# Kernel tuning notes

Measured on AMD Instinct MI355X. Metric: run time of the kernel, lower is better.

## Reference

```python
import jax, jax.numpy as jnp
from jax import lax
import numpy as np

EPS = 1e-5
RADIUS = 0.2
NPOINT = 1024
NSAMPLE = 32
B, N = 8, 8192


def furthest_point_sample(xyz, npoint):
    # xyz: (B,N,3) -> idx (B,npoint), start at index 0 (pytorch3d default)
    Bn, Nn, _ = xyz.shape
    def step(carry, _):
        dists, last = carry  # (B,N), (B,)
        lastpt = jnp.take_along_axis(xyz, last[:, None, None], axis=1)  # (B,1,3)
        d = jnp.sum((xyz - lastpt) ** 2, axis=-1)  # (B,N)
        dists = jnp.minimum(dists, d)
        nxt = jnp.argmax(dists, axis=-1).astype(jnp.int32)
        return (dists, nxt), last
    init = (jnp.full((Bn, Nn), jnp.inf, xyz.dtype), jnp.zeros((Bn,), jnp.int32))
    _, idxs = lax.scan(step, init, None, length=npoint)  # (npoint,B)
    return idxs.T  # (B,npoint)


def ball_query(radius, nsample, xyz, new_xyz):
    # first `nsample` points (by original index order) within radius; pad -> 0 (clamp of -1)
    Nn = xyz.shape[1]
    d2 = jnp.sum((new_xyz[:, :, None, :] - xyz[:, None, :, :]) ** 2, axis=-1)  # (B,S,N)
    valid = d2 < radius * radius
    score = jnp.where(valid, jnp.arange(Nn, dtype=jnp.int32), jnp.int32(Nn))  # smaller = earlier valid
    neg_vals, _ = lax.top_k(-score, nsample)  # picks nsample smallest scores
    idx = -neg_vals  # (B,S,nsample)
    idx = jnp.where(idx == Nn, 0, idx)  # pytorch3d pads with -1, then clamp(min=0) -> 0
    return idx


def bn_relu(x, g, be, m, v):
    # eval-mode BatchNorm over channel (last) dim + ReLU
    return jax.nn.relu((x - m) * (g / jnp.sqrt(v + EPS)) + be)


def setup_inputs() -> dict:
    key = jax.random.key(0)
    ks = jax.random.split(key, 4)
    xyz = jax.random.uniform(ks[0], (B, N, 3), dtype=jnp.float32)
    w1 = jax.random.normal(ks[1], (64, 3), dtype=jnp.float32) * 0.1
    w2 = jax.random.normal(ks[2], (64, 64), dtype=jnp.float32) * 0.1
    w3 = jax.random.normal(ks[3], (128, 64), dtype=jnp.float32) * 0.1
    z64, o64 = jnp.zeros((64,), jnp.float32), jnp.ones((64,), jnp.float32)
    z128, o128 = jnp.zeros((128,), jnp.float32), jnp.ones((128,), jnp.float32)
    return {
        "xyz": xyz,
        "w1": w1, "b1": z64, "g1": o64, "be1": z64, "m1": z64, "v1": o64,
        "w2": w2, "b2": z64, "g2": o64, "be2": z64, "m2": z64, "v2": o64,
        "w3": w3, "b3": z128, "g3": o128, "be3": z128, "m3": z128, "v3": o128,
    }


def reference(xyz, w1, b1, g1, be1, m1, v1, w2, b2, g2, be2, m2, v2, w3, b3, g3, be3, m3, v3):
    fps_idx = furthest_point_sample(xyz, NPOINT)  # (B,npoint)
    new_xyz = jnp.take_along_axis(xyz, fps_idx[:, :, None], axis=1)  # (B,npoint,3)
    idx = ball_query(RADIUS, NSAMPLE, xyz, new_xyz)  # (B,npoint,nsample)
    grouped_xyz = jax.vmap(lambda pts, i: pts[i])(xyz, idx)  # (B,npoint,nsample,3)
    # 1x1 conv MLP (channels-last) + eval BN + ReLU
    h = bn_relu(jnp.einsum('bsnc,oc->bsno', grouped_xyz, w1) + b1, g1, be1, m1, v1)
    h = bn_relu(jnp.einsum('bsnc,oc->bsno', h, w2) + b2, g2, be2, m2, v2)
    h = bn_relu(jnp.einsum('bsnc,oc->bsno', h, w3) + b3, g3, be3, m3, v3)
    new_features = jnp.max(h, axis=2)  # (B,npoint,128) max over nsample
    new_features = jnp.transpose(new_features, (0, 2, 1))  # (B,128,npoint) to match torch layout
    return new_xyz, new_features
```

## Files before the change

kernel.cpp:

```cpp
#include <hip/hip_runtime.h>

#define B 8
#define N 8192
#define S 1024
#define NS 32
#define THREADS 512
#define NCONS_BLK 248
#define NCONS_WAVE (NCONS_BLK * 8)
constexpr float BN_EPS = 1e-5f;

typedef float v2f __attribute__((ext_vector_type(2)));

struct KParams {
  const float* xyz;
  const float *w1, *b1, *g1, *be1, *m1, *v1;
  const float *w2, *b2, *g2, *be2, *m2, *v2;
  const float *w3, *b3, *g3, *be3, *m3, *v3;
  float* new_xyz;
  float* out_feat;
  float* ctrs;
  unsigned* prog;
};

__device__ __forceinline__ float wave_max_to_lane63(float x) {
  int v = __float_as_int(x);
#define DPP_MAX(ctrl)                                                     \
  v = __float_as_int(fmaxf(__int_as_float(v),                             \
      __int_as_float(__builtin_amdgcn_update_dpp(v, v, (ctrl), 0xf, 0xf, \
                                                 false))))
  DPP_MAX(0x111);
  DPP_MAX(0x112);
  DPP_MAX(0x114);
  DPP_MAX(0x118);
  DPP_MAX(0x142);
  DPP_MAX(0x143);
#undef DPP_MAX
  return __int_as_float(v);
}

__device__ __forceinline__ void producer(const KParams& P, char* smem, int b,
                                         int t, int lane, int w) {
#pragma clang fp contract(off)
  float4* s_xyz4 = (float4*)smem;
  float* s_ctr = (float*)(smem + 131072);
  unsigned long long(*s_red)[8] =
      (unsigned long long(*)[8])(smem + 131072 + 12288);
  const float* base = P.xyz + (size_t)b * N * 3;
  v2f X[8], Y[8], Z[8], D[8];
  const int p0 = t * 16;
  {
    const float4* src = (const float4*)(base + (size_t)p0 * 3);
    float buf[48];
#pragma unroll
    for (int i = 0; i < 12; ++i) {
      float4 v = src[i];
      buf[4 * i + 0] = v.x; buf[4 * i + 1] = v.y;
      buf[4 * i + 2] = v.z; buf[4 * i + 3] = v.w;
    }
#pragma unroll
    for (int k = 0; k < 16; ++k)
      s_xyz4[p0 + k] =
          make_float4(buf[3 * k], buf[3 * k + 1], buf[3 * k + 2], 0.f);
#pragma unroll
    for (int i = 0; i < 8; ++i) {
      X[i] = (v2f){buf[6 * i + 0], buf[6 * i + 3]};
      Y[i] = (v2f){buf[6 * i + 1], buf[6 * i + 4]};
      Z[i] = (v2f){buf[6 * i + 2], buf[6 * i + 5]};
      D[i] = (v2f){3.4e38f, 3.4e38f};
    }
  }
  __syncthreads();
  float lx = base[0], ly = base[1], lz = base[2];
  if (t == 0) { s_ctr[0] = lx; s_ctr[1] = ly; s_ctr[2] = lz; }
  for (int r = 1; r < S; ++r) {
    v2f lx2 = lx, ly2 = ly, lz2 = lz;
#pragma unroll
    for (int i = 0; i < 8; ++i) {
      v2f dx = X[i] - lx2, dy = Y[i] - ly2, dz = Z[i] - lz2;
      v2f d = (dx * dx + dy * dy) + dz * dz;
      D[i] = __builtin_elementwise_min(D[i], d);
    }
    float n1[8], n2[4], n3[2];
#pragma unroll
    for (int i = 0; i < 8; ++i) n1[i] = fmaxf(D[i].x, D[i].y);
#pragma unroll
    for (int i = 0; i < 4; ++i) n2[i] = fmaxf(n1[2 * i], n1[2 * i + 1]);
    n3[0] = fmaxf(n2[0], n2[1]);
    n3[1] = fmaxf(n2[2], n2[3]);
    float m = fmaxf(n3[0], n3[1]);
    int c3 = (n3[0] < m) ? 1 : 0;
    float n2s = c3 ? n2[2] : n2[0];
    int c2 = (n2s < m) ? 1 : 0;
    float n1a = c3 ? n1[4] : n1[0];
    float n1b = c3 ? n1[6] : n1[2];
    float n1s = c2 ? n1b : n1a;
    int c1 = (n1s < m) ? 1 : 0;
    float dx0 = c3 ? D[4].x : D[0].x;
    float dx1 = c3 ? D[5].x : D[1].x;
    float dx2 = c3 ? D[6].x : D[2].x;
    float dx3 = c3 ? D[7].x : D[3].x;
    float dxa = c2 ? dx2 : dx0;
    float dxb = c2 ? dx3 : dx1;
    float dxs = c1 ? dxb : dxa;
    int c0 = (dxs < m) ? 1 : 0;
    int li = 8 * c3 + 4 * c2 + 2 * c1 + c0;
    float wm = wave_max_to_lane63(m);
    float wavemax =
        __int_as_float(__builtin_amdgcn_readlane(__float_as_int(wm), 63));
    unsigned long long bal = __ballot(m == wavemax);
    int firstlane = (int)__builtin_ctzll(bal);
    int widx = __builtin_amdgcn_readlane(p0 + li, firstlane);
    unsigned long long key =
        ((unsigned long long)__float_as_uint(wavemax) << 32) |
        (unsigned)(8191 - widx);
    if (lane == 0) s_red[r & 1][w] = key;
    __syncthreads();
    {
      const unsigned long long* sr = s_red[r & 1];
      unsigned long long k0 = sr[0], k1 = sr[1], k2 = sr[2], k3 = sr[3];
      unsigned long long k4 = sr[4], k5 = sr[5], k6 = sr[6], k7 = sr[7];
      unsigned long long a = k0 > k1 ? k0 : k1;
      unsigned long long c = k2 > k3 ? k2 : k3;
      unsigned long long e = k4 > k5 ? k4 : k5;
      unsigned long long g = k6 > k7 ? k6 : k7;
      unsigned long long ac = a > c ? a : c;
      unsigned long long eg = e > g ? e : g;
      unsigned long long kmax = ac > eg ? ac : eg;
      const int bi = 8191 - (int)(unsigned)(kmax & 0xffffffffull);
      float4 cc = s_xyz4[bi];
      lx = cc.x; ly = cc.y; lz = cc.z;
    }
    if (t == 0) {
      s_ctr[r * 3 + 0] = lx; s_ctr[r * 3 + 1] = ly; s_ctr[r * 3 + 2] = lz;
    }
    if (w == 0 && (r & 15) == 15) {
      int k16 = r >> 4;
      if (lane == 0 && k16 >= 1)
        __hip_atomic_store(&P.prog[b * 64], (unsigned)(k16 * 16),
                           __ATOMIC_RELEASE, __HIP_MEMORY_SCOPE_AGENT);
      int cbase = (r - 15) * 3;
      if (lane < 48)
        __hip_atomic_store(P.ctrs + (size_t)b * (S * 3) + cbase + lane,
                           s_ctr[cbase + lane], __ATOMIC_RELAXED,
                           __HIP_MEMORY_SCOPE_AGENT);
    }
  }
  __syncthreads();
  if (w == 0 && lane == 0)
    __hip_atomic_store(&P.prog[b * 64], (unsigned)S, __ATOMIC_RELEASE,
                       __HIP_MEMORY_SCOPE_AGENT);
  float* o = P.new_xyz + (size_t)b * S * 3;
  for (int i = t; i < (S * 3) / 4; i += THREADS)
    ((float4*)o)[i] = ((const float4*)s_ctr)[i];
}

__device__ __forceinline__ void consumer(const KParams& P, char* smem, int cid,
                                         int t, int lane, int w) {
#pragma clang fp contract(off)
  constexpr float R2 = (float)(0.2 * 0.2);
  float* h = (float*)smem + w * (NS * 64);
  float* cs = (float*)smem + 8 * NS * 64 + w * (NS * 4);
  const unsigned gw = cid * 8 + w;
  float sv1 = P.g1[lane] / sqrtf(P.v1[lane] + BN_EPS);
  float bb1 = (P.b1[lane] - P.m1[lane]) * sv1 + P.be1[lane];
  float w1x = P.w1[lane * 3 + 0] * sv1, w1y = P.w1[lane * 3 + 1] * sv1,
        w1z = P.w1[lane * 3 + 2] * sv1;
  float sv2 = P.g2[lane] / sqrtf(P.v2[lane] + BN_EPS);
  float bb2 = (P.b2[lane] - P.m2[lane]) * sv2 + P.be2[lane];
  float W2[64];
#pragma unroll
  for (int k = 0; k < 64; k += 4) {
    float4 q = *(const float4*)(P.w2 + lane * 64 + k);
    W2[k + 0] = q.x * sv2; W2[k + 1] = q.y * sv2;
    W2[k + 2] = q.z * sv2; W2[k + 3] = q.w * sv2;
  }
  float sva = P.g3[lane] / sqrtf(P.v3[lane] + BN_EPS);
  float bba = (P.b3[lane] - P.m3[lane]) * sva + P.be3[lane];
  float svb = P.g3[lane + 64] / sqrtf(P.v3[lane + 64] + BN_EPS);
  float bbb = (P.b3[lane + 64] - P.m3[lane + 64]) * svb + P.be3[lane + 64];
  float Wa[64], Wb[64];
#pragma unroll
  for (int k = 0; k < 64; k += 4) {
    float4 qa = *(const float4*)(P.w3 + lane * 64 + k);
    Wa[k + 0] = qa.x * sva; Wa[k + 1] = qa.y * sva;
    Wa[k + 2] = qa.z * sva; Wa[k + 3] = qa.w * sva;
    float4 qb = *(const float4*)(P.w3 + (lane + 64) * 64 + k);
    Wb[k + 0] = qb.x * svb; Wb[k + 1] = qb.y * svb;
    Wb[k + 2] = qb.z * svb; Wb[k + 3] = qb.w * svb;
  }
  for (unsigned c = gw; c < B * S; c += NCONS_WAVE) {
    const int b = c & 7;
    const int s = c >> 3;
    while (__hip_atomic_load(&P.prog[b * 64], __ATOMIC_RELAXED,
                             __HIP_MEMORY_SCOPE_AGENT) <= (unsigned)s)
      __builtin_amdgcn_s_sleep(8);
    (void)__hip_atomic_load(&P.prog[b * 64], __ATOMIC_ACQUIRE,
                            __HIP_MEMORY_SCOPE_AGENT);
    const float* cg = P.ctrs + (size_t)b * (S * 3) + s * 3;
    float cx = __hip_atomic_load(cg + 0, __ATOMIC_RELAXED,
                                 __HIP_MEMORY_SCOPE_AGENT);
    float cy = __hip_atomic_load(cg + 1, __ATOMIC_RELAXED,
                                 __HIP_MEMORY_SCOPE_AGENT);
    float cz = __hip_atomic_load(cg + 2, __ATOMIC_RELAXED,
                                 __HIP_MEMORY_SCOPE_AGENT);
    const float* base = P.xyz + (size_t)b * N * 3;
    int cnt = 0;
    for (int c0 = 0; c0 < N && cnt < NS; c0 += 64) {
      int p = c0 + lane;
      float x = base[p * 3], y = base[p * 3 + 1], z = base[p * 3 + 2];
      float dx = x - cx, dy = y - cy, dz = z - cz;
      float d = (dx * dx + dy * dy) + dz * dz;
      bool v = d < R2;
      unsigned long long mk = __ballot(v);
      int rank = cnt + __popcll(mk & ((1ull << lane) - 1ull));
      if (v && rank < NS) {
        cs[rank * 4 + 0] = x; cs[rank * 4 + 1] = y; cs[rank * 4 + 2] = z;
      }
      cnt += (int)__popcll(mk);
    }
    if (cnt < NS) {
      float x0 = base[0], y0 = base[1], z0 = base[2];
      for (int j = cnt + lane; j < NS; j += 64) {
        cs[j * 4 + 0] = x0; cs[j * 4 + 1] = y0; cs[j * 4 + 2] = z0;
      }
    }
    for (int n = 0; n < NS; ++n) {
      float a = fmaf(w1x, cs[n * 4 + 0],
                     fmaf(w1y, cs[n * 4 + 1], fmaf(w1z, cs[n * 4 + 2], bb1)));
      h[n * 64 + lane] = fmaxf(a, 0.f);
    }
    for (int n = 0; n < NS; ++n) {
      float acc = bb2;
#pragma unroll
      for (int k = 0; k < 64; k += 4) {
        float4 q = *(const float4*)(h + n * 64 + k);
        acc = fmaf(W2[k + 0], q.x, acc);
        acc = fmaf(W2[k + 1], q.y, acc);
        acc = fmaf(W2[k + 2], q.z, acc);
        acc = fmaf(W2[k + 3], q.w, acc);
      }
      h[n * 64 + lane] = fmaxf(acc, 0.f);
    }
    float mxa = 0.f, mxb = 0.f;
    for (int n = 0; n < NS; ++n) {
      float acca = bba, accb = bbb;
#pragma unroll
      for (int k = 0; k < 64; k += 4) {
        float4 q = *(const float4*)(h + n * 64 + k);
        acca = fmaf(Wa[k + 0], q.x, acca);
        acca = fmaf(Wa[k + 1], q.y, acca);
        acca = fmaf(Wa[k + 2], q.z, acca);
        acca = fmaf(Wa[k + 3], q.w, acca);
        accb = fmaf(Wb[k + 0], q.x, accb);
        accb = fmaf(Wb[k + 1], q.y, accb);
        accb = fmaf(Wb[k + 2], q.z, accb);
        accb = fmaf(Wb[k + 3], q.w, accb);
      }
      mxa = fmaxf(mxa, acca);
      mxb = fmaxf(mxb, accb);
    }
    P.out_feat[((size_t)b * 128 + lane) * S + s] = mxa;
    P.out_feat[((size_t)b * 128 + 64 + lane) * S + s] = mxb;
  }
}

__global__ void __attribute__((amdgpu_flat_work_group_size(THREADS, THREADS),
                               amdgpu_waves_per_eu(2, 2)))
k_fused(KParams P) {
  extern __shared__ char smem[];
  const int t = threadIdx.x;
  const int lane = t & 63;
  const int w = t >> 6;
  if (blockIdx.x < B)
    producer(P, smem, blockIdx.x, t, lane, w);
  else
    consumer(P, smem, blockIdx.x - B, t, lane, w);
}

extern "C" void kernel_launch(void* const* d_in, const int* in_sizes, int n_in,
                              void* d_out, int out_size, void* d_ws,
                              size_t ws_size, hipStream_t stream) {
  KParams P;
  P.xyz = (const float*)d_in[0];
  P.w1 = (const float*)d_in[1];  P.b1 = (const float*)d_in[2];
  P.g1 = (const float*)d_in[3];  P.be1 = (const float*)d_in[4];
  P.m1 = (const float*)d_in[5];  P.v1 = (const float*)d_in[6];
  P.w2 = (const float*)d_in[7];  P.b2 = (const float*)d_in[8];
  P.g2 = (const float*)d_in[9];  P.be2 = (const float*)d_in[10];
  P.m2 = (const float*)d_in[11]; P.v2 = (const float*)d_in[12];
  P.w3 = (const float*)d_in[13]; P.b3 = (const float*)d_in[14];
  P.g3 = (const float*)d_in[15]; P.be3 = (const float*)d_in[16];
  P.m3 = (const float*)d_in[17]; P.v3 = (const float*)d_in[18];
  float* out = (float*)d_out;
  P.new_xyz = out;
  P.out_feat = out + (size_t)B * S * 3;
  P.prog = (unsigned*)d_ws;
  P.ctrs = (float*)((char*)d_ws + 2048);

  hipMemsetAsync(d_ws, 0, 2048, stream);

  dim3 grid(B + NCONS_BLK), blk(THREADS);
  size_t shmem = 131072 + 12288 + 256;
  k_fused<<<grid, blk, shmem, stream>>>(P);
}
```

Measured before the change: 985.1 us.

## Process two batches per FPS producer block, interleaving their argmax chains

Each farthest-point-sampling producer block now handles two batch items at once. The two independent distance-update and argmax chains are interleaved so each block barrier serves both, and four producer blocks replace eight, which frees four more blocks for consumers. The point cloud is no longer staged in LDS; the next centre is read from global memory (likely cache-resident), and centre progress is published every 8 steps instead of every 16 so consumers can start sooner. The cost is roughly double the register pressure in the producer and a dependent global load on the serial critical path.

```diff
diff --git a/kernel.cpp b/kernel.cpp
--- a/kernel.cpp
+++ b/kernel.cpp
@@ -5,7 +5,8 @@
 #define S 1024
 #define NS 32
 #define THREADS 512
-#define NCONS_BLK 248
+#define NPROD_BLK 4
+#define NCONS_BLK 252
 #define NCONS_WAVE (NCONS_BLK * 8)
 constexpr float BN_EPS = 1e-5f;
 
@@ -38,120 +39,181 @@
   return __int_as_float(v);
 }
 
-__device__ __forceinline__ void producer(const KParams& P, char* smem, int b,
+__device__ __forceinline__ void tree16(const v2f D[8], float& m, int& li) {
+  float n1[8], n2[4], n3[2];
+#pragma unroll
+  for (int i = 0; i < 8; ++i) n1[i] = fmaxf(D[i].x, D[i].y);
+#pragma unroll
+  for (int i = 0; i < 4; ++i) n2[i] = fmaxf(n1[2 * i], n1[2 * i + 1]);
+  n3[0] = fmaxf(n2[0], n2[1]);
+  n3[1] = fmaxf(n2[2], n2[3]);
+  m = fmaxf(n3[0], n3[1]);
+  int c3 = (n3[0] < m) ? 1 : 0;
+  float n2s = c3 ? n2[2] : n2[0];
+  int c2 = (n2s < m) ? 1 : 0;
+  float n1a = c3 ? n1[4] : n1[0];
+  float n1b = c3 ? n1[6] : n1[2];
+  float n1s = c2 ? n1b : n1a;
+  int c1 = (n1s < m) ? 1 : 0;
+  float dx0 = c3 ? D[4].x : D[0].x;
+  float dx1 = c3 ? D[5].x : D[1].x;
+  float dx2 = c3 ? D[6].x : D[2].x;
+  float dx3 = c3 ? D[7].x : D[3].x;
+  float dxa = c2 ? dx2 : dx0;
+  float dxb = c2 ? dx3 : dx1;
+  float dxs = c1 ? dxb : dxa;
+  int c0 = (dxs < m) ? 1 : 0;
+  li = 8 * c3 + 4 * c2 + 2 * c1 + c0;
+}
+
+__device__ __forceinline__ void wave_argmax(float m, int p0, int li,
+                                            float& wavemax, int& widx) {
+  float wm = wave_max_to_lane63(m);
+  wavemax = __int_as_float(__builtin_amdgcn_readlane(__float_as_int(wm), 63));
+  unsigned long long bal = __ballot(m == wavemax);
+  int firstlane = (int)__builtin_ctzll(bal);
+  widx = __builtin_amdgcn_readlane(p0 + li, firstlane);
+}
+
+__device__ __forceinline__ void producer(const KParams& P, char* smem, int pb,
                                          int t, int lane, int w) {
 #pragma clang fp contract(off)
-  float4* s_xyz4 = (float4*)smem;
-  float* s_ctr = (float*)(smem + 131072);
-  unsigned long long(*s_red)[8] =
-      (unsigned long long(*)[8])(smem + 131072 + 12288);
-  const float* base = P.xyz + (size_t)b * N * 3;
-  v2f X[8], Y[8], Z[8], D[8];
+  float* s_ctrA = (float*)smem;
+  float* s_ctrB = (float*)(smem + 12288);
+  unsigned long long(*s_redA)[8] =
+      (unsigned long long(*)[8])(smem + 24576);
+  unsigned long long(*s_redB)[8] =
+      (unsigned long long(*)[8])(smem + 24576 + 128);
+  const int bA = 2 * pb, bB = 2 * pb + 1;
+  const float* baseA = P.xyz + (size_t)bA * N * 3;
+  const float* baseB = P.xyz + (size_t)bB * N * 3;
+  v2f XA[8], YA[8], ZA[8], DA[8];
+  v2f XB[8], YB[8], ZB[8], DB[8];
   const int p0 = t * 16;
   {
-    const float4* src = (const float4*)(base + (size_t)p0 * 3);
-    float buf[48];
+    const float4* srcA = (const float4*)(baseA + (size_t)p0 * 3);
+    const float4* srcB = (const float4*)(baseB + (size_t)p0 * 3);
+    float bufA[48], bufB[48];
 #pragma unroll
     for (int i = 0; i < 12; ++i) {
-      float4 v = src[i];
-      buf[4 * i + 0] = v.x; buf[4 * i + 1] = v.y;
-      buf[4 * i + 2] = v.z; buf[4 * i + 3] = v.w;
-    }
-#pragma unroll
-    for (int k = 0; k < 16; ++k)
-      s_xyz4[p0 + k] =
-          make_float4(buf[3 * k], buf[3 * k + 1], buf[3 * k + 2], 0.f);
+      float4 va = srcA[i];
+      bufA[4 * i + 0] = va.x; bufA[4 * i + 1] = va.y;
+      bufA[4 * i + 2] = va.z; bufA[4 * i + 3] = va.w;
+      float4 vb = srcB[i];
+      bufB[4 * i + 0] = vb.x; bufB[4 * i + 1] = vb.y;
+      bufB[4 * i + 2] = vb.z; bufB[4 * i + 3] = vb.w;
+    }
 #pragma unroll
     for (int i = 0; i < 8; ++i) {
-      X[i] = (v2f){buf[6 * i + 0], buf[6 * i + 3]};
-      Y[i] = (v2f){buf[6 * i + 1], buf[6 * i + 4]};
-      Z[i] = (v2f){buf[6 * i + 2], buf[6 * i + 5]};
-      D[i] = (v2f){3.4e38f, 3.4e38f};
-    }
-  }
-  __syncthreads();
-  float lx = base[0], ly = base[1], lz = base[2];
-  if (t == 0) { s_ctr[0] = lx; s_ctr[1] = ly; s_ctr[2] = lz; }
+      XA[i] = (v2f){bufA[6 * i + 0], bufA[6 * i + 3]};
+      YA[i] = (v2f){bufA[6 * i + 1], bufA[6 * i + 4]};
+      ZA[i] = (v2f){bufA[6 * i + 2], bufA[6 * i + 5]};
+      DA[i] = (v2f){3.4e38f, 3.4e38f};
+      XB[i] = (v2f){bufB[6 * i + 0], bufB[6 * i + 3]};
+      YB[i] = (v2f){bufB[6 * i + 1], bufB[6 * i + 4]};
+      ZB[i] = (v2f){bufB[6 * i + 2], bufB[6 * i + 5]};
+      DB[i] = (v2f){3.4e38f, 3.4e38f};
+    }
+  }
+  float lxA = baseA[0], lyA = baseA[1], lzA = baseA[2];
+  float lxB = baseB[0], lyB = baseB[1], lzB = baseB[2];
+  if (w == 0 && lane == 0) { s_ctrA[0] = lxA; s_ctrA[1] = lyA; s_ctrA[2] = lzA; }
+  if (w == 1 && lane == 0) { s_ctrB[0] = lxB; s_ctrB[1] = lyB; s_ctrB[2] = lzB; }
   for (int r = 1; r < S; ++r) {
-    v2f lx2 = lx, ly2 = ly, lz2 = lz;
+    v2f lxA2 = lxA, lyA2 = lyA, lzA2 = lzA;
+    v2f lxB2 = lxB, lyB2 = lyB, lzB2 = lzB;
 #pragma unroll
     for (int i = 0; i < 8; ++i) {
-      v2f dx = X[i] - lx2, dy = Y[i] - ly2, dz = Z[i] - lz2;
-      v2f d = (dx * dx + dy * dy) + dz * dz;
-      D[i] = __builtin_elementwise_min(D[i], d);
-    }
-    float n1[8], n2[4], n3[2];
-#pragma unroll
-    for (int i = 0; i < 8; ++i) n1[i] = fmaxf(D[i].x, D[i].y);
-#pragma unroll
-    for (int i = 0; i < 4; ++i) n2[i] = fmaxf(n1[2 * i], n1[2 * i + 1]);
-    n3[0] = fmaxf(n2[0], n2[1]);
-    n3[1] = fmaxf(n2[2], n2[3]);
-    float m = fmaxf(n3[0], n3[1]);
-    int c3 = (n3[0] < m) ? 1 : 0;
-    float n2s = c3 ? n2[2] : n2[0];
-    int c2 = (n2s < m) ? 1 : 0;
-    float n1a = c3 ? n1[4] : n1[0];
-    float n1b = c3 ? n1[6] : n1[2];
-    float n1s = c2 ? n1b : n1a;
-    int c1 = (n1s < m) ? 1 : 0;
-    float dx0 = c3 ? D[4].x : D[0].x;
-    float dx1 = c3 ? D[5].x : D[1].x;
-    float dx2 = c3 ? D[6].x : D[2].x;
-    float dx3 = c3 ? D[7].x : D[3].x;
-    float dxa = c2 ? dx2 : dx0;
-    float dxb = c2 ? dx3 : dx1;
-    float dxs = c1 ? dxb : dxa;
-    int c0 = (dxs < m) ? 1 : 0;
-    int li = 8 * c3 + 4 * c2 + 2 * c1 + c0;
-    float wm = wave_max_to_lane63(m);
-    float wavemax =
-        __int_as_float(__builtin_amdgcn_readlane(__float_as_int(wm), 63));
-    unsigned long long bal = __ballot(m == wavemax);
-    int firstlane = (int)__builtin_ctzll(bal);
-    int widx = __builtin_amdgcn_readlane(p0 + li, firstlane);
-    unsigned long long key =
-        ((unsigned long long)__float_as_uint(wavemax) << 32) |
-        (unsigned)(8191 - widx);
-    if (lane == 0) s_red[r & 1][w] = key;
+      v2f dxa = XA[i] - lxA2, dya = YA[i] - lyA2, dza = ZA[i] - lzA2;
+      v2f da = (dxa * dxa + dya * dya) + dza * dza;
+      DA[i] = __builtin_elementwise_min(DA[i], da);
+      v2f dxb = XB[i] - lxB2, dyb = YB[i] - lyB2, dzb = ZB[i] - lzB2;
+      v2f db = (dxb * dxb + dyb * dyb) + dzb * dzb;
+      DB[i] = __builtin_elementwise_min(DB[i], db);
+    }
+    float mA, mB;
+    int liA, liB;
+    tree16(DA, mA, liA);
+    tree16(DB, mB, liB);
+    float wavemaxA, wavemaxB;
+    int widxA, widxB;
+    wave_argmax(mA, p0, liA, wavemaxA, widxA);
+    wave_argmax(mB, p0, liB, wavemaxB, widxB);
+    unsigned long long keyA =
+        ((unsigned long long)__float_as_uint(wavemaxA) << 32) |
+        (unsigned)(8191 - widxA);
+    unsigned long long keyB =
+        ((unsigned long long)__float_as_uint(wavemaxB) << 32) |
+        (unsigned)(8191 - widxB);
+    if (lane == 0) {
+      s_redA[r & 1][w] = keyA;
+      s_redB[r & 1][w] = keyB;
+    }
     __syncthreads();
+    int biA, biB;
     {
-      const unsigned long long* sr = s_red[r & 1];
-      unsigned long long k0 = sr[0], k1 = sr[1], k2 = sr[2], k3 = sr[3];
-      unsigned long long k4 = sr[4], k5 = sr[5], k6 = sr[6], k7 = sr[7];
-      unsigned long long a = k0 > k1 ? k0 : k1;
-      unsigned long long c = k2 > k3 ? k2 : k3;
-      unsigned long long e = k4 > k5 ? k4 : k5;
-      unsigned long long g = k6 > k7 ? k6 : k7;
-      unsigned long long ac = a > c ? a : c;
-      unsigned long long eg = e > g ? e : g;
-      unsigned long long kmax = ac > eg ? ac : eg;
-      const int bi = 8191 - (int)(unsigned)(kmax & 0xffffffffull);
-      float4 cc = s_xyz4[bi];
-      lx = cc.x; ly = cc.y; lz = cc.z;
-    }
-    if (t == 0) {
-      s_ctr[r * 3 + 0] = lx; s_ctr[r * 3 + 1] = ly; s_ctr[r * 3 + 2] = lz;
-    }
-    if (w == 0 && (r & 15) == 15) {
-      int k16 = r >> 4;
-      if (lane == 0 && k16 >= 1)
-        __hip_atomic_store(&P.prog[b * 64], (unsigned)(k16 * 16),
+      const unsigned long long* sa = s_redA[r & 1];
+      const unsigned long long* sb = s_redB[r & 1];
+      unsigned long long a0 = sa[0], a1 = sa[1], a2 = sa[2], a3 = sa[3];
+      unsigned long long a4 = sa[4], a5 = sa[5], a6 = sa[6], a7 = sa[7];
+      unsigned long long b0 = sb[0], b1 = sb[1], b2 = sb[2], b3 = sb[3];
+      unsigned long long b4 = sb[4], b5 = sb[5], b6 = sb[6], b7 = sb[7];
+      unsigned long long pa = a0 > a1 ? a0 : a1;
+      unsigned long long qa = a2 > a3 ? a2 : a3;
+      unsigned long long ra = a4 > a5 ? a4 : a5;
+      unsigned long long sa2 = a6 > a7 ? a6 : a7;
+      unsigned long long ta = pa > qa ? pa : qa;
+      unsigned long long ua = ra > sa2 ? ra : sa2;
+      unsigned long long ka = ta > ua ? ta : ua;
+      biA = 8191 - (int)(unsigned)(ka & 0xffffffffull);
+      unsigned long long pb2 = b0 > b1 ? b0 : b1;
+      unsigned long long qb = b2 > b3 ? b2 : b3;
+      unsigned long long rb = b4 > b5 ? b4 : b5;
+      unsigned long long sb2 = b6 > b7 ? b6 : b7;
+      unsigned long long tb = pb2 > qb ? pb2 : qb;
+      unsigned long long ub = rb > sb2 ? rb : sb2;
+      unsigned long long kb = tb > ub ? tb : ub;
+      biB = 8191 - (int)(unsigned)(kb & 0xffffffffull);
+    }
+    const float* cpA = baseA + (size_t)biA * 3;
+    const float* cpB = baseB + (size_t)biB * 3;
+    float nlxA = cpA[0], nlyA = cpA[1], nlzA = cpA[2];
+    float nlxB = cpB[0], nlyB = cpB[1], nlzB = cpB[2];
+    lxA = nlxA; lyA = nlyA; lzA = nlzA;
+    lxB = nlxB; lyB = nlyB; lzB = nlzB;
+    if (w == 0 && lane == 0) {
+      s_ctrA[r * 3 + 0] = lxA; s_ctrA[r * 3 + 1] = lyA; s_ctrA[r * 3 + 2] = lzA;
+    }
+    if (w == 1 && lane == 0) {
+      s_ctrB[r * 3 + 0] = lxB; s_ctrB[r * 3 + 1] = lyB; s_ctrB[r * 3 + 2] = lzB;
+    }
+    if ((r & 7) == 7 && w < 2) {
+      const int bb = (w == 0) ? bA : bB;
+      const float* sc = (w == 0) ? s_ctrA : s_ctrB;
+      int k8 = r >> 3;
+      if (lane == 0 && k8 >= 1)
+        __hip_atomic_store(&P.prog[bb * 64], (unsigned)(k8 * 8),
                            __ATOMIC_RELEASE, __HIP_MEMORY_SCOPE_AGENT);
-      int cbase = (r - 15) * 3;
-      if (lane < 48)
-        __hip_atomic_store(P.ctrs + (size_t)b * (S * 3) + cbase + lane,
-                           s_ctr[cbase + lane], __ATOMIC_RELAXED,
+      int cbase = (r - 7) * 3;
+      if (lane < 24)
+        __hip_atomic_store(P.ctrs + (size_t)bb * (S * 3) + cbase + lane,
+                           sc[cbase + lane], __ATOMIC_RELAXED,
                            __HIP_MEMORY_SCOPE_AGENT);
     }
   }
   __syncthreads();
   if (w == 0 && lane == 0)
-    __hip_atomic_store(&P.prog[b * 64], (unsigned)S, __ATOMIC_RELEASE,
+    __hip_atomic_store(&P.prog[bA * 64], (unsigned)S, __ATOMIC_RELEASE,
                        __HIP_MEMORY_SCOPE_AGENT);
-  float* o = P.new_xyz + (size_t)b * S * 3;
-  for (int i = t; i < (S * 3) / 4; i += THREADS)
-    ((float4*)o)[i] = ((const float4*)s_ctr)[i];
+  if (w == 1 && lane == 0)
+    __hip_atomic_store(&P.prog[bB * 64], (unsigned)S, __ATOMIC_RELEASE,
+                       __HIP_MEMORY_SCOPE_AGENT);
+  float* oA = P.new_xyz + (size_t)bA * S * 3;
+  float* oB = P.new_xyz + (size_t)bB * S * 3;
+  for (int i = t; i < (S * 3) / 4; i += THREADS) {
+    ((float4*)oA)[i] = ((const float4*)s_ctrA)[i];
+    ((float4*)oB)[i] = ((const float4*)s_ctrB)[i];
+  }
 }
 
 __device__ __forceinline__ void consumer(const KParams& P, char* smem, int cid,
@@ -271,10 +333,10 @@
   const int t = threadIdx.x;
   const int lane = t & 63;
   const int w = t >> 6;
-  if (blockIdx.x < B)
+  if (blockIdx.x < NPROD_BLK)
     producer(P, smem, blockIdx.x, t, lane, w);
   else
-    consumer(P, smem, blockIdx.x - B, t, lane, w);
+    consumer(P, smem, blockIdx.x - NPROD_BLK, t, lane, w);
 }
 
 extern "C" void kernel_launch(void* const* d_in, const int* in_sizes, int n_in,
@@ -299,7 +361,7 @@
 
   hipMemsetAsync(d_ws, 0, 2048, stream);
 
-  dim3 grid(B + NCONS_BLK), blk(THREADS);
-  size_t shmem = 131072 + 12288 + 256;
+  dim3 grid(NPROD_BLK + NCONS_BLK), blk(THREADS);
+  size_t shmem = 86016;
   k_fused<<<grid, blk, shmem, stream>>>(P);
 }
```

New measurement: 1.873 ms. 1.9x slower.
